# Kernel tuning notes

Hardware: AMD Instinct MI355X
Metric: run time of the kernel (lower is better)

## Reference

```python
import jax, jax.numpy as jnp
import numpy as np
from math import sqrt

NUM_HEADS = 16
DIM_MODEL = 1024


def setup_inputs() -> dict:
    key = jax.random.key(0)
    ks = jax.random.split(key, 12)
    B, S, D, M = 4, 1024, DIM_MODEL, 64
    bound = 1.0 / sqrt(D)
    def lin_w(k):
        return jax.random.uniform(k, (D, D), jnp.float32, -bound, bound)
    def lin_b(k):
        return jax.random.uniform(k, (D,), jnp.float32, -bound, bound)
    return {
        "query": jax.random.normal(ks[0], (B, S, D), jnp.float32),
        "key": jax.random.normal(ks[1], (B, S, D), jnp.float32),
        "value": jax.random.normal(ks[2], (B, S, D), jnp.float32),
        "mask": jax.random.randint(ks[3], (1, B, S, M), 0, 2).astype(jnp.float32),
        "Wq": lin_w(ks[4]), "bq": lin_b(ks[5]),
        "Wk": lin_w(ks[6]), "bk": lin_b(ks[7]),
        "Wv": lin_w(ks[8]), "bv": lin_b(ks[9]),
        "Wo": lin_w(ks[10]),
    }


def reference(query, key, value, mask, Wq, bq, Wk, bk, Wv, bv, Wo):
    B, S, D = query.shape
    H = NUM_HEADS
    d = D // H
    # projections + head split, permute(2,0,1,3) -> [H,B,S,d]
    q = (query @ Wq.T + bq).reshape(B, S, H, d).transpose(2, 0, 1, 3)
    k = (key @ Wk.T + bk).reshape(B, S, H, d).transpose(2, 0, 1, 3)
    v = (value @ Wv.T + bv).reshape(B, S, H, d).transpose(2, 0, 1, 3)
    attn = jnp.einsum("hbqd,hbkd->hbqk", q, k) / sqrt(d)  # [H,B,S,S]
    # custom mask: mask.repeat(H,1,1,1) then mask @ mask^T / sqrt(m).
    # Identical per-head, so compute once on [B,S,m] and broadcast over H.
    m2d = mask[0]  # [B,S,m]
    mm = jnp.einsum("bqm,bkm->bqk", m2d, m2d) / sqrt(m2d.shape[-1])
    attn = jnp.where(mm[None] == 0, jnp.float32(-1e9), attn)
    w = jax.nn.softmax(attn, axis=-1)  # dropout is identity in eval mode
    x = jnp.einsum("hbqk,hbkd->hbqd", w, v)  # [H,B,S,d]
    # torch: permute(1,2,0,3) -> [B,S,H,d]; transpose(1,2) -> [B,H,S,d];
    # contiguous().view(B,-1,H*d) -- row-major reshape (mixes head/seq layout, replicated faithfully)
    x = jnp.transpose(x, (1, 0, 2, 3))  # [B,H,S,d]
    x = x.reshape(B, -1, H * d)
    return x @ Wo.T
```

## Files before the change

### kernel.cpp

```cpp
#include <hip/hip_runtime.h>

typedef unsigned int u32;
typedef unsigned short u16;
typedef unsigned long long u64;
typedef __attribute__((ext_vector_type(8))) short s16x8;
typedef __attribute__((ext_vector_type(8))) __bf16 bf16x8;
typedef __attribute__((ext_vector_type(4))) float f32x4;
typedef __attribute__((ext_vector_type(16))) float f32x16;
typedef __attribute__((ext_vector_type(4))) u32 u32x4;

#define WSMB (1ull << 20)
#define QSC 0.18033688011112042f

static __device__ __forceinline__ u16 f2bf(float f) {
  u32 u = __builtin_bit_cast(u32, f);
  return (u16)((u + 0x7fffu + ((u >> 16) & 1u)) >> 16);
}

static __device__ __forceinline__ u32 pkbf(float lo, float hi) {
  u32 r;
  asm("v_cvt_pk_bf16_f32 %0, %1, %2" : "=v"(r) : "v"(lo), "v"(hi));
  return r;
}

static __device__ __forceinline__ float ex2(float x) {
  float r;
  asm("v_exp_f32 %0, %1" : "=v"(r) : "v"(x));
  return r;
}

static __device__ __forceinline__ f32x4 mfma16x16(s16x8 a, s16x8 b, f32x4 c) {
  return __builtin_amdgcn_mfma_f32_16x16x32_bf16(
      __builtin_bit_cast(bf16x8, a), __builtin_bit_cast(bf16x8, b), c, 0, 0, 0);
}

static __device__ __forceinline__ f32x16 mfma32x32(s16x8 a, s16x8 b, f32x16 c) {
  return __builtin_amdgcn_mfma_f32_32x32x16_bf16(
      __builtin_bit_cast(bf16x8, a), __builtin_bit_cast(bf16x8, b), c, 0, 0, 0);
}

#define GLOAD_LDS16(g, l)                                                      \
  __builtin_amdgcn_global_load_lds(                                            \
      (const __attribute__((address_space(1))) u32*)(const void*)(g),          \
      (__attribute__((address_space(3))) u32*)(void*)(l), 16, 0, 0)

__global__ __launch_bounds__(256) void k_prep(
    const float* __restrict__ xq, const float* __restrict__ xk,
    const float* __restrict__ xv, const float* __restrict__ wq,
    const float* __restrict__ wk, const float* __restrict__ wv,
    const float* __restrict__ wo, const float* __restrict__ mask,
    u16* __restrict__ oxq, u16* __restrict__ oxk, u16* __restrict__ oxv,
    u16* __restrict__ owq, u16* __restrict__ owk, u16* __restrict__ owv,
    u16* __restrict__ owo, u64* __restrict__ bits) {
  const int y = blockIdx.y;
  if (y >= 3 && blockIdx.x >= 1024) return;
  if (y == 7) {
    int w = threadIdx.x >> 6, l = threadIdx.x & 63;
    int r = blockIdx.x * 4 + w;
    float v = mask[(size_t)r * 64 + l];
    u64 bl = __ballot(v != 0.0f);
    if (l == 0) bits[r] = bl;
    return;
  }
  const float* s;
  u16* d;
  switch (y) {
    case 0: s = xq; d = oxq; break;
    case 1: s = xk; d = oxk; break;
    case 2: s = xv; d = oxv; break;
    case 3: s = wq; d = owq; break;
    case 4: s = wk; d = owk; break;
    case 5: s = wv; d = owv; break;
    default: s = wo; d = owo; break;
  }
  int i = (blockIdx.x * 256 + threadIdx.x) * 4;
  float4 v = *(const float4*)(s + i);
  u64 p = (u64)f2bf(v.x) | ((u64)f2bf(v.y) << 16) | ((u64)f2bf(v.z) << 32) |
          ((u64)f2bf(v.w) << 48);
  *(u64*)(d + i) = p;
}

__global__ __launch_bounds__(256) void k_mm(const u64* __restrict__ bits,
                                            u64* __restrict__ MB) {
  int wv = threadIdx.x >> 6, l = threadIdx.x & 63;
  int qg = blockIdx.x * 4 + wv;
  u64 bq = bits[qg];
  const u64* bb = bits + (qg & ~1023);
  u64* out = MB + (size_t)qg * 16;
  for (int kt = 0; kt < 16; kt++) {
    u64 bk = bb[kt * 64 + l];
    u64 m = __ballot((bq & bk) != 0ull);
    if (l == 0) out[kt] = m;
  }
}

static __device__ __forceinline__ void gemm_core(const u16* __restrict__ A,
                                                 const u16* __restrict__ Bw,
                                                 f32x4 (&acc)[4][4]) {
  __shared__ __attribute__((aligned(16))) u16 As[2][4096];
  __shared__ __attribute__((aligned(16))) u16 Bs[2][4096];
  const int t = threadIdx.x;
  const int l = t & 63, w = t >> 6, lr = l & 15, lk = l >> 4;
  const int amr = (w & 1) * 64, bnr = (w >> 1) * 64;
  const int c0 = t, c1 = t + 256;
  const int r0 = c0 >> 2, r1 = c1 >> 2;
  const int sw0 = ((c0 & 3) * 8) ^ ((r0 & 6) << 2);
  const int sw1 = ((c1 & 3) * 8) ^ ((r1 & 6) << 2);
  const u16* Ag0 = A + (size_t)r0 * 1024 + sw0;
  const u16* Ag1 = A + (size_t)r1 * 1024 + sw1;
  const u16* Bg0 = Bw + (size_t)r0 * 1024 + sw0;
  const u16* Bg1 = Bw + (size_t)r1 * 1024 + sw1;
  const int aswz = (lk * 16) ^ ((lr & 6) << 3);

  GLOAD_LDS16(Ag0, &As[0][c0 * 8]);
  GLOAD_LDS16(Ag1, &As[0][c1 * 8]);
  GLOAD_LDS16(Bg0, &Bs[0][c0 * 8]);
  GLOAD_LDS16(Bg1, &Bs[0][c1 * 8]);

  int cur = 0;
  for (int kt = 0; kt < 1024; kt += 32) {
    __syncthreads();
    if (kt < 992) {
      const int nxt = cur ^ 1;
      GLOAD_LDS16(Ag0 + kt + 32, &As[nxt][c0 * 8]);
      GLOAD_LDS16(Ag1 + kt + 32, &As[nxt][c1 * 8]);
      GLOAD_LDS16(Bg0 + kt + 32, &Bs[nxt][c0 * 8]);
      GLOAD_LDS16(Bg1 + kt + 32, &Bs[nxt][c1 * 8]);
    }
    const char* Ac = (const char*)As[cur];
    const char* Bc = (const char*)Bs[cur];
    s16x8 af[4], bf[4];
#pragma unroll
    for (int i = 0; i < 4; i++)
      af[i] = *(const s16x8*)(Ac + (amr + i * 16 + lr) * 64 + aswz);
#pragma unroll
    for (int j = 0; j < 4; j++)
      bf[j] = *(const s16x8*)(Bc + (bnr + j * 16 + lr) * 64 + aswz);
    __builtin_amdgcn_s_setprio(1);
#pragma unroll
    for (int i = 0; i < 4; i++)
#pragma unroll
      for (int j = 0; j < 4; j++)
        acc[i][j] = mfma16x16(af[i], bf[j], acc[i][j]);
    __builtin_amdgcn_s_setprio(0);
    cur ^= 1;
  }
}

__global__ __launch_bounds__(256) void k_qkv(
    const u16* __restrict__ Xq, const u16* __restrict__ Xk,
    const u16* __restrict__ Xv, const u16* __restrict__ Wqb,
    const u16* __restrict__ Wkb, const u16* __restrict__ Wvb,
    const float* __restrict__ bq, const float* __restrict__ bk,
    const float* __restrict__ bv, u16* __restrict__ Qo, u16* __restrict__ Ko,
    u16* __restrict__ V4) {
  const int bid0 = blockIdx.x;
  const int bid = (bid0 & 7) * 96 + (bid0 >> 3);
  const int proj = bid >> 8;
  const int rem = bid & 255;
  const int st = rem >> 3, dt = rem & 7;
  const u16* Xp = proj == 0 ? Xq : (proj == 1 ? Xk : Xv);
  const u16* Wp = proj == 0 ? Wqb : (proj == 1 ? Wkb : Wvb);
  const float* bias = proj == 0 ? bq : (proj == 1 ? bk : bv);
  const int t = threadIdx.x;
  const int l = t & 63, w = t >> 6, lr = l & 15, lk = l >> 4;
  const int amr = (w & 1) * 64, bnr = (w >> 1) * 64;
  f32x4 acc[4][4] = {};
  if (proj < 2) {
    const float sc = proj == 0 ? QSC : 1.0f;
    gemm_core(Wp + (size_t)dt * 131072, Xp + (size_t)st * 131072, acc);
    u16* O = proj ? Ko : Qo;
#pragma unroll
    for (int i = 0; i < 4; i++) {
      const int d0 = dt * 128 + amr + i * 16 + lk * 4;
      const int h = d0 >> 6, dd0 = d0 & 63;
      const float4 b4 = *(const float4*)(bias + d0);
#pragma unroll
      for (int j = 0; j < 4; j++) {
        const int s = st * 128 + bnr + j * 16 + lr;
        const int b_ = s >> 10, si = s & 1023;
        u32 e0 = pkbf((acc[i][j][0] + b4.x) * sc, (acc[i][j][1] + b4.y) * sc);
        u32 e1 = pkbf((acc[i][j][2] + b4.z) * sc, (acc[i][j][3] + b4.w) * sc);
        *(u64*)(O + ((size_t)((b_ * 16 + h) * 1024 + si)) * 64 + dd0) =
            (u64)e0 | ((u64)e1 << 32);
      }
    }
  } else {
    gemm_core(Xp + (size_t)st * 131072, Wp + (size_t)dt * 131072, acc);
#pragma unroll
    for (int i = 0; i < 4; i++) {
      const int s0 = st * 128 + amr + i * 16 + lk * 4;
      const int b_ = s0 >> 10, si = s0 & 1023;
      const int sblk = si >> 3, soff = si & 7;
#pragma unroll
      for (int j = 0; j < 4; j++) {
        const int d = dt * 128 + bnr + j * 16 + lr;
        const int h = d >> 6, dd = d & 63;
        const float bb = bias[d];
        u32 e0 = pkbf(acc[i][j][0] + bb, acc[i][j][1] + bb);
        u32 e1 = pkbf(acc[i][j][2] + bb, acc[i][j][3] + bb);
        *(u64*)(V4 + (size_t)(b_ * 16 + h) * 65536 +
                (size_t)(sblk * 64 + dd) * 8 + soff) =
            (u64)e0 | ((u64)e1 << 32);
      }
    }
  }
}

__global__ __launch_bounds__(256) void k_oproj(const u16* __restrict__ Xb,
                                               const u16* __restrict__ Wob,
                                               float* __restrict__ Out) {
  const int bid0 = blockIdx.x;
  const int bid = (bid0 & 7) * 32 + (bid0 >> 3);
  const int mb = bid >> 3, nb = bid & 7;
  f32x4 acc[4][4] = {};
  gemm_core(Xb + (size_t)mb * 131072, Wob + (size_t)nb * 131072, acc);
  const int t = threadIdx.x;
  const int l = t & 63, w = t >> 6, lr = l & 15, lk = l >> 4;
  const int amr = (w & 1) * 64, bnr = (w >> 1) * 64;
#pragma unroll
  for (int i = 0; i < 4; i++)
#pragma unroll
    for (int j = 0; j < 4; j++)
#pragma unroll
      for (int r = 0; r < 4; r++) {
        const int m = mb * 128 + amr + i * 16 + lk * 4 + r;
        const int n = nb * 128 + bnr + j * 16 + lr;
        Out[(size_t)m * 1024 + n] = acc[i][j][r];
      }
}

__global__ __launch_bounds__(128, 2) void k_attn(const u16* __restrict__ Qb,
                                                 const u16* __restrict__ Kb,
                                                 const u16* __restrict__ V4,
                                                 const u64* __restrict__ MB,
                                                 u16* __restrict__ xbuf) {
  const int t = threadIdx.x, l = t & 63, w = t >> 6;
  const int q5 = l & 31, hi = l >> 5;
  const int bid = (blockIdx.x & 7) * 128 + (blockIdx.x >> 3);
  const int qt = bid & 15, hb = bid >> 4;
  const int h = hb >> 2, b = hb & 3;
  const int s0 = qt * 64;
  const u16* Qhb = Qb + (size_t)(b * 16 + h) * 65536;
  const u16* Khb = Kb + (size_t)(b * 16 + h) * 65536;
  const u16* Vhb = V4 + (size_t)(b * 16 + h) * 65536;
  const int q = s0 + w * 32 + q5;
  const u64* MBq = MB + ((size_t)b * 1024 + q) * 16;

  s16x8 qf[4];
#pragma unroll
  for (int ds = 0; ds < 4; ds++)
    qf[ds] = *(const s16x8*)(Qhb + (size_t)q * 64 + ds * 16 + hi * 8);

  f32x16 xa0 = {}, xa1 = {};
  float ls = 0.f, m_ = -__builtin_inff();

  const u16* Kr0 = Khb + (size_t)q5 * 64 + hi * 8;
  const u16* Kr1 = Khb + (size_t)(32 + q5) * 64 + hi * 8;
  const u16* Vr0 = Vhb + (size_t)q5 * 8;
  const u16* Vr1 = Vhb + (size_t)(32 + q5) * 8;

  u64 mw = MBq[0];
  for (int kt = 0; kt < 16; kt++) {
    const int ko = kt * 4096;
    const int vb = kt * 8 + hi;
    s16x8 k0[4], k1[4];
#pragma unroll
    for (int ds = 0; ds < 4; ds++) {
      k0[ds] = *(const s16x8*)(Kr0 + ko + ds * 16);
      k1[ds] = *(const s16x8*)(Kr1 + ko + ds * 16);
    }
    s16x8 v0[4], v1[4];
#pragma unroll
    for (int ks = 0; ks < 4; ks++) {
      v0[ks] = *(const s16x8*)(Vr0 + (size_t)(vb + 2 * ks) * 512);
      v1[ks] = *(const s16x8*)(Vr1 + (size_t)(vb + 2 * ks) * 512);
    }
    const u64 nw = MBq[(kt + 1) & 15];

    f32x16 z0 = {}, z1 = {};
    __builtin_amdgcn_s_setprio(1);
#pragma unroll
    for (int ds = 0; ds < 4; ds++) {
      z0 = mfma32x32(k0[ds], qf[ds], z0);
      z1 = mfma32x32(k1[ds], qf[ds], z1);
    }
    __builtin_amdgcn_s_setprio(0);

    float tmx[16];
#pragma unroll
    for (int r = 0; r < 16; r++) tmx[r] = fmaxf(z0[r], z1[r]);
#pragma unroll
    for (int st_ = 8; st_ >= 1; st_ >>= 1)
#pragma unroll
      for (int r = 0; r < 8; r++)
        if (r < st_) tmx[r] = fmaxf(tmx[r], tmx[r + st_]);
    float tm = tmx[0];
    tm = fmaxf(tm, __shfl_xor(tm, 32));
    if (tm > m_) {
      const float scl = ex2(m_ - tm);
      m_ = tm;
      ls *= scl;
      xa0 *= scl;
      xa1 *= scl;
    }

    float e0[16], e1[16];
#pragma unroll
    for (int r = 0; r < 16; r++) e0[r] = ex2(z0[r] - m_);
#pragma unroll
    for (int r = 0; r < 16; r++) e1[r] = ex2(z1[r] - m_);
    if (!__all(mw == ~0ull)) {
      const u32 mh0 = (u32)(mw >> (hi * 4));
      const u32 mh1 = (u32)(mw >> (hi * 4 + 32));
#pragma unroll
      for (int r = 0; r < 16; r++) {
        const int bp = 8 * (r >> 2) + (r & 3);
        e0[r] = ((mh0 >> bp) & 1u) ? e0[r] : 0.f;
        e1[r] = ((mh1 >> bp) & 1u) ? e1[r] : 0.f;
      }
    }
    float ts = 0.f;
#pragma unroll
    for (int r = 0; r < 16; r++) ts += e0[r] + e1[r];
    ls += ts;

    u32 P0[2][4], P1[2][4];
#pragma unroll
    for (int qi = 0; qi < 4; qi++) {
      P0[0][qi] = pkbf(e0[4 * qi], e0[4 * qi + 1]);
      P1[0][qi] = pkbf(e0[4 * qi + 2], e0[4 * qi + 3]);
      P0[1][qi] = pkbf(e1[4 * qi], e1[4 * qi + 1]);
      P1[1][qi] = pkbf(e1[4 * qi + 2], e1[4 * qi + 3]);
    }

#pragma unroll
    for (int ks = 0; ks < 4; ks++) {
      const int kb_ = ks >> 1, qi0 = (ks & 1) * 2, qi1 = qi0 + 1;
      u32 w0 = P0[kb_][qi0], w2 = P0[kb_][qi1];
      u32 w1 = P1[kb_][qi0], w3 = P1[kb_][qi1];
      asm("v_permlane32_swap_b32 %0, %1" : "+v"(w0), "+v"(w2));
      asm("v_permlane32_swap_b32 %0, %1" : "+v"(w1), "+v"(w3));
      u32x4 fv;
      fv[0] = w0; fv[1] = w1; fv[2] = w2; fv[3] = w3;
      const s16x8 pb = __builtin_bit_cast(s16x8, fv);
      __builtin_amdgcn_s_setprio(1);
      xa0 = mfma32x32(v0[ks], pb, xa0);
      xa1 = mfma32x32(v1[ks], pb, xa1);
      __builtin_amdgcn_s_setprio(0);
    }
    mw = nw;
  }

  ls += __shfl_xor(ls, 32);
  const float inv = 1.0f / ls;
  const size_t rowb = (size_t)b * 1048576 + (size_t)(h * 64 + (q >> 4)) * 1024 +
                      (size_t)(q & 15) * 64;
#pragma unroll
  for (int qi = 0; qi < 4; qi++) {
    u32 a0 = pkbf(xa0[4 * qi] * inv, xa0[4 * qi + 1] * inv);
    u32 a1 = pkbf(xa0[4 * qi + 2] * inv, xa0[4 * qi + 3] * inv);
    *(u64*)(xbuf + rowb + 8 * qi + 4 * hi) = (u64)a0 | ((u64)a1 << 32);
    u32 b0 = pkbf(xa1[4 * qi] * inv, xa1[4 * qi + 1] * inv);
    u32 b1 = pkbf(xa1[4 * qi + 2] * inv, xa1[4 * qi + 3] * inv);
    *(u64*)(xbuf + rowb + 32 + 8 * qi + 4 * hi) = (u64)b0 | ((u64)b1 << 32);
  }
}

extern "C" void kernel_launch(void* const* d_in, const int* in_sizes, int n_in,
                              void* d_out, int out_size, void* d_ws,
                              size_t ws_size, hipStream_t stream) {
  const float* query = (const float*)d_in[0];
  const float* key_ = (const float*)d_in[1];
  const float* value = (const float*)d_in[2];
  const float* mask = (const float*)d_in[3];
  const float* bq = (const float*)d_in[5];
  const float* bk = (const float*)d_in[7];
  const float* bv = (const float*)d_in[9];
  const float* Wq = (const float*)d_in[4];
  const float* Wk = (const float*)d_in[6];
  const float* Wv = (const float*)d_in[8];
  const float* Wo = (const float*)d_in[10];

  char* ws = (char*)d_ws;
  u16* Xq = (u16*)(ws + 0 * WSMB);
  u16* Xk = (u16*)(ws + 8 * WSMB);
  u16* Xv = (u16*)(ws + 16 * WSMB);
  u16* Wqb = (u16*)(ws + 24 * WSMB);
  u16* Wkb = (u16*)(ws + 26 * WSMB);
  u16* Wvb = (u16*)(ws + 28 * WSMB);
  u16* Wob = (u16*)(ws + 30 * WSMB);
  u16* Qb = (u16*)(ws + 32 * WSMB);
  u16* Kb = (u16*)(ws + 40 * WSMB);
  u16* V4 = (u16*)(ws + 48 * WSMB);
  u64* bits = (u64*)(ws + 56 * WSMB);
  u64* MBm = (u64*)(ws + 8 * WSMB);
  u16* xbuf = Xq;

  k_prep<<<dim3(4096, 8), 256, 0, stream>>>(query, key_, value, Wq, Wk, Wv, Wo,
                                            mask, Xq, Xk, Xv, Wqb, Wkb, Wvb,
                                            Wob, bits);
  k_qkv<<<768, 256, 0, stream>>>(Xq, Xk, Xv, Wqb, Wkb, Wvb, bq, bk, bv, Qb, Kb,
                                 V4);
  k_mm<<<1024, 256, 0, stream>>>(bits, MBm);
  k_attn<<<1024, 128, 0, stream>>>(Qb, Kb, V4, MBm, xbuf);
  k_oproj<<<256, 256, 0, stream>>>(xbuf, Wob, (float*)d_out);
}
```

Measured before the change: 129.4 us.

## Split attention key range across two wave pairs and merge partial softmax via LDS

```diff
diff --git a/kernel.cpp b/kernel.cpp
--- a/kernel.cpp
+++ b/kernel.cpp
@@ -230,13 +230,16 @@
       }
 }
 
-__global__ __launch_bounds__(128, 2) void k_attn(const u16* __restrict__ Qb,
+__global__ __launch_bounds__(256, 4) void k_attn(const u16* __restrict__ Qb,
                                                  const u16* __restrict__ Kb,
                                                  const u16* __restrict__ V4,
                                                  const u64* __restrict__ MB,
                                                  u16* __restrict__ xbuf) {
+  __shared__ __attribute__((aligned(16))) float cmb[128 * 36];
   const int t = threadIdx.x, l = t & 63, w = t >> 6;
   const int q5 = l & 31, hi = l >> 5;
+  const int wq = w & 1;
+  const int kh = w >> 1;
   const int bid = (blockIdx.x & 7) * 128 + (blockIdx.x >> 3);
   const int qt = bid & 15, hb = bid >> 4;
   const int h = hb >> 2, b = hb & 3;
@@ -244,8 +247,9 @@
   const u16* Qhb = Qb + (size_t)(b * 16 + h) * 65536;
   const u16* Khb = Kb + (size_t)(b * 16 + h) * 65536;
   const u16* Vhb = V4 + (size_t)(b * 16 + h) * 65536;
-  const int q = s0 + w * 32 + q5;
+  const int q = s0 + wq * 32 + q5;
   const u64* MBq = MB + ((size_t)b * 1024 + q) * 16;
+  const int kt0 = kh * 8;
 
   s16x8 qf[4];
 #pragma unroll
@@ -260,8 +264,9 @@
   const u16* Vr0 = Vhb + (size_t)q5 * 8;
   const u16* Vr1 = Vhb + (size_t)(32 + q5) * 8;
 
-  u64 mw = MBq[0];
-  for (int kt = 0; kt < 16; kt++) {
+  u64 mw = MBq[kt0];
+  for (int i = 0; i < 8; i++) {
+    const int kt = kt0 + i;
     const int ko = kt * 4096;
     const int vb = kt * 8 + hi;
     s16x8 k0[4], k1[4];
@@ -276,7 +281,7 @@
       v0[ks] = *(const s16x8*)(Vr0 + (size_t)(vb + 2 * ks) * 512);
       v1[ks] = *(const s16x8*)(Vr1 + (size_t)(vb + 2 * ks) * 512);
     }
-    const u64 nw = MBq[(kt + 1) & 15];
+    const u64 nw = MBq[kt0 + ((i + 1) & 7)];
 
     f32x16 z0 = {}, z1 = {};
     __builtin_amdgcn_s_setprio(1);
@@ -350,6 +355,27 @@
       __builtin_amdgcn_s_setprio(0);
     }
     mw = nw;
+  }
+
+  if (w >= 2) {
+    float* p = &cmb[(size_t)((w - 2) * 64 + l) * 36];
+    *(f32x16*)(p) = xa0;
+    *(f32x16*)(p + 16) = xa1;
+    p[32] = m_;
+    p[33] = ls;
+  }
+  __syncthreads();
+  if (w >= 2) return;
+  {
+    const float* p = &cmb[(size_t)(wq * 64 + l) * 36];
+    const f32x16 xb0 = *(const f32x16*)(p);
+    const f32x16 xb1 = *(const f32x16*)(p + 16);
+    const float mb = p[32], lsb = p[33];
+    const float m = fmaxf(m_, mb);
+    const float sa = ex2(m_ - m), sb = ex2(mb - m);
+    ls = ls * sa + lsb * sb;
+    xa0 = xa0 * sa + xb0 * sb;
+    xa1 = xa1 * sa + xb1 * sb;
   }
 
   ls += __shfl_xor(ls, 32);
@@ -403,6 +429,6 @@
   k_qkv<<<768, 256, 0, stream>>>(Xq, Xk, Xv, Wqb, Wkb, Wvb, bq, bk, bv, Qb, Kb,
                                  V4);
   k_mm<<<1024, 256, 0, stream>>>(bits, MBm);
-  k_attn<<<1024, 128, 0, stream>>>(Qb, Kb, V4, MBm, xbuf);
+  k_attn<<<1024, 256, 0, stream>>>(Qb, Kb, V4, MBm, xbuf);
   k_oproj<<<256, 256, 0, stream>>>(xbuf, Wob, (float*)d_out);
 }
```

New measurement: 170.2 us. 1.32x slower.
